# Performance work log

Measured on AMD Instinct MI355X. Metric: run time of the kernel, lower is better.

Reference implementation:

```python
import jax, jax.numpy as jnp
import numpy as np
from jax import lax

DIM = 256
HEADS = 8
P = 4  # split_size (patch_size)
SCALE = (DIM // HEADS) ** -0.5  # note: scale uses full head_dim = dim//heads, per the torch code


def _win(t, p1, p2, h):
    # 'b (h d) (gx p1) (gy p2) -> (b gx gy) h (p1 p2) d'
    b, c, X, Y = t.shape
    d = c // h
    gx, gy = X // p1, Y // p2
    t = t.reshape(b, h, d, gx, p1, gy, p2).transpose(0, 3, 5, 1, 4, 6, 2)
    return t.reshape(b * gx * gy, h, p1 * p2, d)


def _unwin(v, b, gx, gy, h, p1, p2):
    # '(b gx gy) h (p1 p2) d -> b (h d) (gx p1) (gy p2)'
    d = v.shape[-1]
    v = v.reshape(b, gx, gy, h, p1, p2, d).transpose(0, 3, 6, 1, 4, 2, 5)
    return v.reshape(b, h * d, gx * p1, gy * p2)


def _conv(x, w, stride):
    return lax.conv_general_dilated(x, w, stride, 'VALID',
                                    dimension_numbers=('NCHW', 'OIHW', 'NCHW'))


def _attn_branch(q, k, v, lepe):
    # q: (G,h,Nq,d), k/lepe: (G,h,Nk,d), v: (G,h,Nq,d)
    attn = jax.nn.softmax((q * SCALE) @ jnp.swapaxes(k, -2, -1), axis=-1)  # (G,h,Nq,Nk)
    # torch does attn.transpose(-2,-1) @ v + lepe -> output indexed by key tokens
    return jnp.einsum('ghqk,ghqd->ghkd', attn, v) + lepe


def setup_inputs() -> dict:
    key = jax.random.key(0)
    ks = jax.random.split(key, 6)
    b, x, y = 16, 64, 64
    fmap = jax.random.normal(ks[0], (b, DIM, x, y), dtype=jnp.float32)
    W_qvh = jax.random.normal(ks[1], (DIM, DIM // 2, 2, 1), dtype=jnp.float32) * 0.02
    W_qvv = jax.random.normal(ks[2], (DIM, DIM // 2, 1, 2), dtype=jnp.float32) * 0.02
    W_k = jax.random.normal(ks[3], (DIM, DIM), dtype=jnp.float32) * 0.02
    W_lepe = jax.random.normal(ks[4], (DIM, DIM), dtype=jnp.float32) * 0.02
    W_proj = jax.random.normal(ks[5], (DIM, DIM), dtype=jnp.float32) * 0.02
    return {"fmap": fmap, "W_qvh": W_qvh, "W_qvv": W_qvv,
            "W_k": W_k, "W_lepe": W_lepe, "W_proj": W_proj}


def reference(fmap, W_qvh, W_qvv, W_k, W_lepe, W_proj):
    b, n, x, y = fmap.shape
    h, p = HEADS, P
    half = n // 2
    # strided qv projections (size=0 path)
    qv_h = _conv(fmap[:, :half], W_qvh, (2, 1))  # (b, n, x/2, y)
    qv_v = _conv(fmap[:, half:], W_qvv, (1, 2))  # (b, n, x, y/2)
    # 1x1 convs as channel matmuls
    k_all = jnp.einsum('bcxy,oc->boxy', fmap, W_k)
    lepe_all = jnp.einsum('bcxy,oc->boxy', fmap, W_lepe)

    # horizontal branch: strips of width p spanning full height
    q_h = _win(qv_h[:, :half], x // 2, p, h)     # (b*(y/p), h, (x/2)*p, d)
    v_h = _win(qv_h[:, half:], x // 2, p, h)
    k_h = _win(k_all[:, :half], x, p, h)         # (b*(y/p), h, x*p, d)
    lepe_h = _win(lepe_all[:, :half], x, p, h)
    out_h = _attn_branch(q_h, k_h, v_h, lepe_h)  # (b*(y/p), h, x*p, d)
    out_h = _unwin(out_h, b, 1, y // p, h, x, p)  # (b, n/2, x, y)

    # vertical branch: strips of height p spanning full width
    q_v = _win(qv_v[:, :half], p, y // 2, h)
    v_v = _win(qv_v[:, half:], p, y // 2, h)
    k_v = _win(k_all[:, half:], p, y, h)
    lepe_v = _win(lepe_all[:, half:], p, y, h)
    out_v = _attn_branch(q_v, k_v, v_v, lepe_v)
    out_v = _unwin(out_v, b, x // p, 1, h, p, y)  # (b, n/2, x, y)

    cat = jnp.concatenate([out_h, out_v], axis=1)  # (b, n, x, y)
    return fmap + jnp.einsum('bcxy,oc->boxy', cat, W_proj)
```

## Files before the change

### kernel.cpp

```cpp
#include <hip/hip_runtime.h>
#include <hip/hip_bf16.h>

#define QSC 0.25503533f

typedef unsigned short bfu;
typedef unsigned int u32;
typedef __attribute__((ext_vector_type(8))) short bf8v;
typedef __attribute__((ext_vector_type(4))) float f32x4;
typedef __attribute__((ext_vector_type(8))) unsigned short u16x8;
typedef __attribute__((ext_vector_type(4))) unsigned int u32x4;

__device__ __forceinline__ bfu f2b(float x) {
    __hip_bfloat16 h = __float2bfloat16(x);
    return *(bfu*)&h;
}
__device__ __forceinline__ float bu2f(bfu u) {
    return __uint_as_float(((unsigned int)u) << 16);
}
__device__ __forceinline__ u32 cvtpk(float lo, float hi) {
    u32 r;
    asm("v_cvt_pk_bf16_f32 %0, %1, %2" : "=v"(r) : "v"(lo), "v"(hi));
    return r;
}
__device__ __forceinline__ void gload16(const bfu* g, bfu* l) {
    __builtin_amdgcn_global_load_lds(
        (const __attribute__((address_space(1))) unsigned int*)g,
        (__attribute__((address_space(3))) unsigned int*)l, 16, 0, 0);
}

__global__ __launch_bounds__(256) void k_prep_f(const float* __restrict__ fmap,
                                                bfu* __restrict__ Fbf) {
    const int x = blockIdx.x, b = blockIdx.y;
    const int t = threadIdx.x;
    __shared__ float tile[64][69];
    for (int cc = 0; cc < 256; cc += 64) {
        #pragma unroll
        for (int i = 0; i < 4; ++i) {
            const int c = (t >> 4) + i * 16, y4 = (t & 15) * 4;
            const float4 v = *(const float4*)(fmap + (((size_t)b * 256 + cc + c) * 64 + x) * 64 + y4);
            tile[y4][c] = v.x; tile[y4 + 1][c] = v.y; tile[y4 + 2][c] = v.z; tile[y4 + 3][c] = v.w;
        }
        __syncthreads();
        const int y = t >> 2, cs = (t & 3) * 16;
        u16x8 o0, o1;
        #pragma unroll
        for (int j = 0; j < 8; ++j) { o0[j] = f2b(tile[y][cs + j]); o1[j] = f2b(tile[y][cs + 8 + j]); }
        bfu* dst = Fbf + (((size_t)b * 64 + x) * 64 + y) * 256 + cc + cs;
        *(u16x8*)dst = o0; *(u16x8*)(dst + 8) = o1;
        __syncthreads();
    }
}

__global__ __launch_bounds__(256) void k_prep_w(
    const float* __restrict__ Wk, const float* __restrict__ Wl,
    const float* __restrict__ Wh, const float* __restrict__ Wv,
    bfu* __restrict__ Wkl, bfu* __restrict__ Whr, bfu* __restrict__ Wvr) {
    const int i = blockIdx.x * 256 + threadIdx.x;
    {
        const int o = i >> 8;
        Wkl[i] = f2b((o < 256) ? Wk[i] : Wl[i - 65536]);
    }
    if (i < 65536) {
        const int o = i >> 8, r = i & 255, kh = r >> 7, c = r & 127;
        const int s = (o * 128 + c) * 2 + kh;
        Whr[i] = f2b(Wh[s]);
        Wvr[i] = f2b(Wv[s]);
    }
}

template<int MODE>
__global__ __launch_bounds__(512) void k_gemm(
    const bfu* __restrict__ Ab16, const float* __restrict__ Af32,
    const bfu* __restrict__ Bsrc,
    bfu* __restrict__ o_kall, bfu* __restrict__ o_lepe, bfu* __restrict__ o_qv,
    const float* __restrict__ resid, float* __restrict__ outf) {
    const int ng = blockIdx.x, mt = blockIdx.y, b = blockIdx.z;
    const int m0 = mt * 128;
    const int t = threadIdx.x, lane = t & 63;
    const int wave = t >> 6;
    const int wm = wave >> 1, wn = wave & 1;
    const int lq = lane >> 4, lr = lane & 15;
    __shared__ bfu Bs[2][64 * 256];
    const bfu* fb = Bsrc + (size_t)b * 1048576;

    bf8v af[8][2];
    if (MODE == 3) {
        #pragma unroll
        for (int k0 = 0; k0 < 8; ++k0)
            #pragma unroll
            for (int mi = 0; mi < 2; ++mi) {
                const float* ap = Af32 + (size_t)(m0 + wm * 32 + mi * 16 + lr) * 256 + k0 * 32 + lq * 8;
                const float4 u0 = *(const float4*)ap;
                const float4 u1 = *(const float4*)(ap + 4);
                bf8v a;
                a[0] = (short)f2b(u0.x); a[1] = (short)f2b(u0.y);
                a[2] = (short)f2b(u0.z); a[3] = (short)f2b(u0.w);
                a[4] = (short)f2b(u1.x); a[5] = (short)f2b(u1.y);
                a[6] = (short)f2b(u1.z); a[7] = (short)f2b(u1.w);
                af[k0][mi] = a;
            }
    } else {
        #pragma unroll
        for (int k0 = 0; k0 < 8; ++k0)
            #pragma unroll
            for (int mi = 0; mi < 2; ++mi)
                af[k0][mi] = *(const bf8v*)(Ab16 + (size_t)(m0 + wm * 32 + mi * 16 + lr) * 256 + k0 * 32 + lq * 8);
    }

    auto stage = [&](int buf, int nt) {
        const int n0 = nt * 64;
        const int lrow = lane >> 5, c1 = lane & 31;
        #pragma unroll
        for (int i = 0; i < 4; ++i) {
            const int row = wave * 8 + i * 2 + lrow;
            const int cS = c1 ^ (row & 7);
            int so;
            if (MODE == 0 || MODE == 3) {
                so = (n0 + row) * 256 + cS * 8;
            } else if (MODE == 1) {
                const int n = n0 + row;
                const int xo = n >> 6, y = n & 63;
                so = ((2 * xo + (cS >> 4)) * 64 + y) * 256 + (cS & 15) * 8;
            } else {
                const int n = n0 + row;
                const int x = n >> 5, yo = n & 31;
                so = (x * 64 + 2 * yo + (cS >> 4)) * 256 + 128 + (cS & 15) * 8;
            }
            gload16(fb + so, &Bs[buf][(wave * 8 + i * 2) * 256]);
        }
    };

    const int nt0 = ng * 4;
    stage(0, nt0);
    __syncthreads();

    for (int tt = 0; tt < 4; ++tt) {
        if (tt + 1 < 4) stage((tt + 1) & 1, nt0 + tt + 1);

        const int buf = tt & 1;
        f32x4 acc[2][2];
        #pragma unroll
        for (int mi = 0; mi < 2; ++mi)
            #pragma unroll
            for (int ni = 0; ni < 2; ++ni) {
                acc[mi][ni][0] = 0.f; acc[mi][ni][1] = 0.f;
                acc[mi][ni][2] = 0.f; acc[mi][ni][3] = 0.f;
            }
        #pragma unroll
        for (int k0 = 0; k0 < 8; ++k0) {
            bf8v bv[2];
            #pragma unroll
            for (int ni = 0; ni < 2; ++ni) {
                const int row = wn * 32 + ni * 16 + lr;
                const int ck = (k0 * 4 + lq) ^ (row & 7);
                bv[ni] = *(const bf8v*)(&Bs[buf][row * 256 + ck * 8]);
            }
            #pragma unroll
            for (int mi = 0; mi < 2; ++mi)
                #pragma unroll
                for (int ni = 0; ni < 2; ++ni)
                    acc[mi][ni] = __builtin_amdgcn_mfma_f32_16x16x32_bf16(af[k0][mi], bv[ni], acc[mi][ni], 0, 0, 0);
        }

        const int n0 = (nt0 + tt) * 64;
        if (MODE == 0) {
            bfu* outp = (mt < 2) ? o_kall : o_lepe;
            const int chb = (mt & 1) * 128 + wm * 32;
            #pragma unroll
            for (int mi = 0; mi < 2; ++mi)
                #pragma unroll
                for (int ni = 0; ni < 2; ++ni) {
                    const int ch = chb + mi * 16 + lq * 4;
                    const int ngl = n0 + wn * 32 + ni * 16 + lr;
                    ushort4 pk;
                    pk.x = f2b(acc[mi][ni][0]); pk.y = f2b(acc[mi][ni][1]);
                    pk.z = f2b(acc[mi][ni][2]); pk.w = f2b(acc[mi][ni][3]);
                    *(ushort4*)(outp + ((size_t)b * 4096 + ngl) * 256 + ch) = pk;
                }
        } else if (MODE == 1 || MODE == 2) {
            const float qs = (mt == 0) ? QSC : 1.0f;
            #pragma unroll
            for (int mi = 0; mi < 2; ++mi)
                #pragma unroll
                for (int ni = 0; ni < 2; ++ni) {
                    const int ch = m0 + wm * 32 + mi * 16 + lq * 4;
                    const int ngl = n0 + wn * 32 + ni * 16 + lr;
                    ushort4 pk;
                    pk.x = f2b(acc[mi][ni][0] * qs); pk.y = f2b(acc[mi][ni][1] * qs);
                    pk.z = f2b(acc[mi][ni][2] * qs); pk.w = f2b(acc[mi][ni][3] * qs);
                    *(ushort4*)(o_qv + ((size_t)b * 2048 + ngl) * 256 + ch) = pk;
                }
        } else {
            #pragma unroll
            for (int mi = 0; mi < 2; ++mi)
                #pragma unroll
                for (int ni = 0; ni < 2; ++ni) {
                    const int ngl = n0 + wn * 32 + ni * 16 + lr;
                    #pragma unroll
                    for (int r = 0; r < 4; ++r) {
                        const int m = m0 + wm * 32 + mi * 16 + lq * 4 + r;
                        const size_t ad = ((size_t)b * 256 + m) * 4096 + ngl;
                        outf[ad] = resid[ad] + acc[mi][ni][r];
                    }
                }
        }
        if (tt + 1 < 4) __syncthreads();
    }
}

template<int BR>
__global__ __launch_bounds__(256) void k_attn(
    const bfu* __restrict__ Qv, const bfu* __restrict__ Kb,
    const bfu* __restrict__ Lp, bfu* __restrict__ cat) {
    const int bid = blockIdx.x;
    const int h = (bid >> 8) & 7;
    const int bg = bid & 255;
    const int b = bg >> 4, g = bg & 15;
    const int t = threadIdx.x, lane = t & 63, w = t >> 6;
    const int lr = lane & 15, lq = lane >> 4;
    const int chQ = h * 16, chV = 128 + h * 16;
    const int chO = (BR == 0) ? h * 16 : 128 + h * 16;
    const bfu* Qb = Qv + (size_t)b * 2048 * 256;
    const bfu* Kg = Kb + (size_t)b * 4096 * 256 + chO;
    const bfu* Lg = Lp + (size_t)b * 4096 * 256 + chO;
    bfu* Cg = cat + (size_t)b * 4096 * 256 + chO;

    __shared__ __align__(16) bfu q_lds[128 * 16];
    __shared__ __align__(16) bfu v_lds[128 * 16];
    __shared__ float psum[2][256];

    {
        const int tok = (w << 5) + (lane >> 1), half = lane & 1;
        const int sp = (BR == 0) ? ((tok >> 2) * 64 + g * 4 + (tok & 3))
                                 : ((g * 4 + (tok >> 5)) * 32 + (tok & 31));
        gload16(Qb + (size_t)sp * 256 + chQ + half * 8, q_lds + w * 512);
        gload16(Qb + (size_t)sp * 256 + chV + half * 8, v_lds + w * 512);
    }

    bf8v kf[4];
    #pragma unroll
    for (int ct = 0; ct < 4; ++ct) {
        const int ktok = (4 * w + ct) * 16 + lr;
        const int sp = (BR == 0) ? ((ktok >> 2) * 64 + g * 4 + (ktok & 3))
                                 : ((g * 4 + (ktok >> 6)) * 64 + (ktok & 63));
        if (lq < 2) kf[ct] = *(const bf8v*)(Kg + (size_t)sp * 256 + lq * 8);
        else        kf[ct] = bf8v{0, 0, 0, 0, 0, 0, 0, 0};
    }
    __syncthreads();

    f32x4 oacc[4];
    #pragma unroll
    for (int ct = 0; ct < 4; ++ct) { oacc[ct][0] = 0.f; oacc[ct][1] = 0.f; oacc[ct][2] = 0.f; oacc[ct][3] = 0.f; }

    for (int gq = 0; gq < 2; ++gq) {
        bf8v qf[4];
        #pragma unroll
        for (int qt = 0; qt < 4; ++qt) {
            const int qtok = gq * 64 + qt * 16 + lr;
            if (lq < 2) qf[qt] = *(const bf8v*)(q_lds + qtok * 16 + lq * 8);
            else        qf[qt] = bf8v{0, 0, 0, 0, 0, 0, 0, 0};
        }
        bf8v vf[2];
        #pragma unroll
        for (int c = 0; c < 2; ++c)
            #pragma unroll
            for (int j = 0; j < 8; ++j)
                vf[c][j] = (short)v_lds[(gq * 64 + c * 32 + lq * 8 + j) * 16 + lr];

        f32x4 acc[4][4];
        #pragma unroll
        for (int qt = 0; qt < 4; ++qt)
            #pragma unroll
            for (int ct = 0; ct < 4; ++ct) {
                acc[qt][ct][0] = 0.f; acc[qt][ct][1] = 0.f; acc[qt][ct][2] = 0.f; acc[qt][ct][3] = 0.f;
            }
        #pragma unroll
        for (int qt = 0; qt < 4; ++qt)
            #pragma unroll
            for (int ct = 0; ct < 4; ++ct)
                acc[qt][ct] = __builtin_amdgcn_mfma_f32_16x16x32_bf16(qf[qt], kf[ct], acc[qt][ct], 0, 0, 0);

        #pragma unroll
        for (int qt = 0; qt < 4; ++qt)
            #pragma unroll
            for (int ct = 0; ct < 4; ++ct)
                #pragma unroll
                for (int r = 0; r < 4; ++r)
                    acc[qt][ct][r] = exp2f(acc[qt][ct][r]);

        float rr[4][4];
        #pragma unroll
        for (int qt = 0; qt < 4; ++qt)
            #pragma unroll
            for (int r = 0; r < 4; ++r)
                rr[qt][r] = (acc[qt][0][r] + acc[qt][1][r]) + (acc[qt][2][r] + acc[qt][3][r]);
        #pragma unroll
        for (int s = 1; s <= 8; s <<= 1)
            #pragma unroll
            for (int qt = 0; qt < 4; ++qt)
                #pragma unroll
                for (int r = 0; r < 4; ++r)
                    rr[qt][r] += __shfl_xor(rr[qt][r], s);
        if (lr == 0) {
            #pragma unroll
            for (int qt = 0; qt < 4; ++qt)
                #pragma unroll
                for (int r = 0; r < 4; ++r)
                    psum[gq][w * 64 + qt * 16 + lq * 4 + r] = rr[qt][r];
        }
        __syncthreads();
        float inv[4][4];
        #pragma unroll
        for (int qt = 0; qt < 4; ++qt)
            #pragma unroll
            for (int r = 0; r < 4; ++r) {
                const int qi = qt * 16 + lq * 4 + r;
                inv[qt][r] = 1.0f / ((psum[gq][qi] + psum[gq][64 + qi]) +
                                     (psum[gq][128 + qi] + psum[gq][192 + qi]));
            }

        u32 pk[4][4][2];
        #pragma unroll
        for (int qt = 0; qt < 4; ++qt)
            #pragma unroll
            for (int ct = 0; ct < 4; ++ct) {
                pk[qt][ct][0] = cvtpk(acc[qt][ct][0] * inv[qt][0], acc[qt][ct][1] * inv[qt][1]);
                pk[qt][ct][1] = cvtpk(acc[qt][ct][2] * inv[qt][2], acc[qt][ct][3] * inv[qt][3]);
            }

        const int base = ((lane >> 4) & 1) * 32 + (lane & 15);
        const bool hi = (lq >= 2);
        #pragma unroll
        for (int c = 0; c < 2; ++c) {
            #pragma unroll
            for (int ct = 0; ct < 4; ++ct) {
                const u32 a0 = (u32)__shfl((int)pk[2 * c][ct][0], base);
                const u32 a1 = (u32)__shfl((int)pk[2 * c][ct][1], base);
                const u32 a2 = (u32)__shfl((int)pk[2 * c][ct][0], base + 16);
                const u32 a3 = (u32)__shfl((int)pk[2 * c][ct][1], base + 16);
                const u32 b0 = (u32)__shfl((int)pk[2 * c + 1][ct][0], base);
                const u32 b1 = (u32)__shfl((int)pk[2 * c + 1][ct][1], base);
                const u32 b2 = (u32)__shfl((int)pk[2 * c + 1][ct][0], base + 16);
                const u32 b3 = (u32)__shfl((int)pk[2 * c + 1][ct][1], base + 16);
                u32x4 wd;
                wd[0] = hi ? b0 : a0; wd[1] = hi ? b1 : a1;
                wd[2] = hi ? b2 : a2; wd[3] = hi ? b3 : a3;
                const bf8v pf = __builtin_bit_cast(bf8v, wd);
                oacc[ct] = __builtin_amdgcn_mfma_f32_16x16x32_bf16(vf[c], pf, oacc[ct], 0, 0, 0);
            }
        }
    }

    #pragma unroll
    for (int ct = 0; ct < 4; ++ct) {
        const int ktok = (4 * w + ct) * 16 + lr;
        const int sp = (BR == 0) ? ((ktok >> 2) * 64 + g * 4 + (ktok & 3))
                                 : ((g * 4 + (ktok >> 6)) * 64 + (ktok & 63));
        const size_t off = (size_t)sp * 256 + lq * 4;
        const ushort4 l4 = *(const ushort4*)(Lg + off);
        ushort4 o;
        o.x = f2b(oacc[ct][0] + bu2f(l4.x));
        o.y = f2b(oacc[ct][1] + bu2f(l4.y));
        o.z = f2b(oacc[ct][2] + bu2f(l4.z));
        o.w = f2b(oacc[ct][3] + bu2f(l4.w));
        *(ushort4*)(Cg + off) = o;
    }
}

extern "C" void kernel_launch(void* const* d_in, const int* in_sizes, int n_in,
                              void* d_out, int out_size, void* d_ws, size_t ws_size,
                              hipStream_t stream) {
    const float* fmap = (const float*)d_in[0];
    const float* Wqvh = (const float*)d_in[1];
    const float* Wqvv = (const float*)d_in[2];
    const float* Wk   = (const float*)d_in[3];
    const float* Wl   = (const float*)d_in[4];
    const float* Wp   = (const float*)d_in[5];
    float* out = (float*)d_out;
    char* ws = (char*)d_ws;

    bfu* Fbf   = (bfu*)(ws);
    bfu* cat   = Fbf;
    bfu* k_all = (bfu*)(ws + 33554432);
    bfu* lepe  = (bfu*)(ws + 67108864);
    bfu* qvh   = (bfu*)(ws + 100663296);
    bfu* qvv   = (bfu*)(ws + 117440512);

    bfu* Wkl = (bfu*)d_out;
    bfu* Whr = (bfu*)((char*)d_out + 262144);
    bfu* Wvr = (bfu*)((char*)d_out + 393216);

    k_prep_f<<<dim3(64, 16), 256, 0, stream>>>(fmap, Fbf);
    k_prep_w<<<dim3(512), 256, 0, stream>>>(Wk, Wl, Wqvh, Wqvv, Wkl, Whr, Wvr);
    k_gemm<0><<<dim3(16, 4, 16), 512, 0, stream>>>(Wkl, nullptr, Fbf, k_all, lepe, nullptr, nullptr, nullptr);
    k_gemm<1><<<dim3(8, 2, 16), 512, 0, stream>>>(Whr, nullptr, Fbf, nullptr, nullptr, qvh, nullptr, nullptr);
    k_gemm<2><<<dim3(8, 2, 16), 512, 0, stream>>>(Wvr, nullptr, Fbf, nullptr, nullptr, qvv, nullptr, nullptr);
    k_attn<0><<<dim3(2048), 256, 0, stream>>>(qvh, k_all, lepe, cat);
    k_attn<1><<<dim3(2048), 256, 0, stream>>>(qvv, k_all, lepe, cat);
    k_gemm<3><<<dim3(16, 2, 16), 512, 0, stream>>>(nullptr, Wp, cat, nullptr, nullptr, nullptr, fmap, out);
}
```

Baseline: 233.2 us.

## Run attention blocks as single wavefronts with K staged in LDS

The attention kernel now uses one 64-thread wavefront per (batch, strip, head) instead of four. Each wave loads all 256 keys into LDS and loops over 8 query groups of 16, keeping 16 output accumulators. This removes the cross-wave softmax partial-sum exchange and its block barriers, and trims the wasted lane work in the P·V MFMA packing. In exchange, each block does four times the serial work, register pressure rises from holding 16 score tiles, and the number of waves in flight drops.

Measured after the change: 216.7 us. 1.08x faster.

```diff
diff --git a/kernel.cpp b/kernel.cpp
--- a/kernel.cpp
+++ b/kernel.cpp
@@ -209,14 +209,14 @@
 }
 
 template<int BR>
-__global__ __launch_bounds__(256) void k_attn(
+__global__ __launch_bounds__(64, 2) void k_attn(
     const bfu* __restrict__ Qv, const bfu* __restrict__ Kb,
     const bfu* __restrict__ Lp, bfu* __restrict__ cat) {
     const int bid = blockIdx.x;
-    const int h = (bid >> 8) & 7;
+    const int h = bid >> 8;
     const int bg = bid & 255;
     const int b = bg >> 4, g = bg & 15;
-    const int t = threadIdx.x, lane = t & 63, w = t >> 6;
+    const int lane = threadIdx.x;
     const int lr = lane & 15, lq = lane >> 4;
     const int chQ = h * 16, chV = 128 + h * 16;
     const int chO = (BR == 0) ? h * 16 : 128 + h * 16;
@@ -225,135 +225,101 @@
     const bfu* Lg = Lp + (size_t)b * 4096 * 256 + chO;
     bfu* Cg = cat + (size_t)b * 4096 * 256 + chO;
 
-    __shared__ __align__(16) bfu q_lds[128 * 16];
-    __shared__ __align__(16) bfu v_lds[128 * 16];
-    __shared__ float psum[2][256];
+    __shared__ __align__(16) bfu q_lds[2048];
+    __shared__ __align__(16) bfu v_lds[2048];
+    __shared__ __align__(16) bfu k_lds[4096];
 
     {
-        const int tok = (w << 5) + (lane >> 1), half = lane & 1;
-        const int sp = (BR == 0) ? ((tok >> 2) * 64 + g * 4 + (tok & 3))
-                                 : ((g * 4 + (tok >> 5)) * 32 + (tok & 31));
-        gload16(Qb + (size_t)sp * 256 + chQ + half * 8, q_lds + w * 512);
-        gload16(Qb + (size_t)sp * 256 + chV + half * 8, v_lds + w * 512);
-    }
-
-    bf8v kf[4];
+        const int half = lane & 1;
+        #pragma unroll
+        for (int c = 0; c < 4; ++c) {
+            const int tok = c * 32 + (lane >> 1);
+            const int sp = (BR == 0) ? ((tok >> 2) * 64 + g * 4 + (tok & 3))
+                                     : ((g * 4 + (tok >> 5)) * 32 + (tok & 31));
+            gload16(Qb + (size_t)sp * 256 + chQ + half * 8, q_lds + c * 512);
+            gload16(Qb + (size_t)sp * 256 + chV + half * 8, v_lds + c * 512);
+        }
+        #pragma unroll
+        for (int c = 0; c < 8; ++c) {
+            const int ktok = c * 32 + (lane >> 1);
+            const int sp = (BR == 0) ? ((ktok >> 2) * 64 + g * 4 + (ktok & 3))
+                                     : ((g * 4 + (ktok >> 6)) * 64 + (ktok & 63));
+            gload16(Kg + (size_t)sp * 256 + half * 8, k_lds + c * 512);
+        }
+    }
+    __syncthreads();
+
+    const bf8v zero8 = {0, 0, 0, 0, 0, 0, 0, 0};
+    const f32x4 zero4 = {0.f, 0.f, 0.f, 0.f};
+    const bool hi = (lq >= 2);
+    const int base = (lq & 1) * 32 + lr;
+
+    f32x4 oacc[16];
     #pragma unroll
-    for (int ct = 0; ct < 4; ++ct) {
-        const int ktok = (4 * w + ct) * 16 + lr;
-        const int sp = (BR == 0) ? ((ktok >> 2) * 64 + g * 4 + (ktok & 3))
-                                 : ((g * 4 + (ktok >> 6)) * 64 + (ktok & 63));
-        if (lq < 2) kf[ct] = *(const bf8v*)(Kg + (size_t)sp * 256 + lq * 8);
-        else        kf[ct] = bf8v{0, 0, 0, 0, 0, 0, 0, 0};
-    }
-    __syncthreads();
-
-    f32x4 oacc[4];
+    for (int ct = 0; ct < 16; ++ct) {
+        oacc[ct][0] = 0.f; oacc[ct][1] = 0.f; oacc[ct][2] = 0.f; oacc[ct][3] = 0.f;
+    }
+
+    for (int qg = 0; qg < 8; ++qg) {
+        const bf8v qf = hi ? zero8 : *(const bf8v*)(q_lds + (qg * 16 + lr) * 16 + lq * 8);
+        bf8v vf;
+        #pragma unroll
+        for (int j = 0; j < 8; ++j)
+            vf[j] = (short)v_lds[(qg * 16 + (lq & 1) * 8 + j) * 16 + lr];
+
+        f32x4 acc[16];
+        #pragma unroll
+        for (int ct = 0; ct < 16; ++ct) {
+            const bf8v kf = hi ? zero8 : *(const bf8v*)(k_lds + (ct * 16 + lr) * 16 + lq * 8);
+            acc[ct] = __builtin_amdgcn_mfma_f32_16x16x32_bf16(qf, kf, zero4, 0, 0, 0);
+        }
+
+        #pragma unroll
+        for (int ct = 0; ct < 16; ++ct)
+            #pragma unroll
+            for (int r = 0; r < 4; ++r)
+                acc[ct][r] = exp2f(acc[ct][r]);
+
+        float rr[4];
+        #pragma unroll
+        for (int r = 0; r < 4; ++r) {
+            float s = 0.f;
+            #pragma unroll
+            for (int ct = 0; ct < 16; ++ct) s += acc[ct][r];
+            rr[r] = s;
+        }
+        #pragma unroll
+        for (int s = 1; s <= 8; s <<= 1)
+            #pragma unroll
+            for (int r = 0; r < 4; ++r)
+                rr[r] += __shfl_xor(rr[r], s);
+        float inv[4];
+        #pragma unroll
+        for (int r = 0; r < 4; ++r) inv[r] = 1.0f / rr[r];
+
+        u32 pk[16][2];
+        #pragma unroll
+        for (int ct = 0; ct < 16; ++ct) {
+            pk[ct][0] = cvtpk(acc[ct][0] * inv[0], acc[ct][1] * inv[1]);
+            pk[ct][1] = cvtpk(acc[ct][2] * inv[2], acc[ct][3] * inv[3]);
+        }
+        #pragma unroll
+        for (int ct = 0; ct < 16; ++ct) {
+            const u32 a0 = (u32)__shfl((int)pk[ct][0], base);
+            const u32 a1 = (u32)__shfl((int)pk[ct][1], base);
+            const u32 a2 = (u32)__shfl((int)pk[ct][0], base + 16);
+            const u32 a3 = (u32)__shfl((int)pk[ct][1], base + 16);
+            u32x4 wd;
+            wd[0] = hi ? 0u : a0; wd[1] = hi ? 0u : a1;
+            wd[2] = hi ? 0u : a2; wd[3] = hi ? 0u : a3;
+            const bf8v pf = __builtin_bit_cast(bf8v, wd);
+            oacc[ct] = __builtin_amdgcn_mfma_f32_16x16x32_bf16(vf, pf, oacc[ct], 0, 0, 0);
+        }
+    }
+
     #pragma unroll
-    for (int ct = 0; ct < 4; ++ct) { oacc[ct][0] = 0.f; oacc[ct][1] = 0.f; oacc[ct][2] = 0.f; oacc[ct][3] = 0.f; }
-
-    for (int gq = 0; gq < 2; ++gq) {
-        bf8v qf[4];
-        #pragma unroll
-        for (int qt = 0; qt < 4; ++qt) {
-            const int qtok = gq * 64 + qt * 16 + lr;
-            if (lq < 2) qf[qt] = *(const bf8v*)(q_lds + qtok * 16 + lq * 8);
-            else        qf[qt] = bf8v{0, 0, 0, 0, 0, 0, 0, 0};
-        }
-        bf8v vf[2];
-        #pragma unroll
-        for (int c = 0; c < 2; ++c)
-            #pragma unroll
-            for (int j = 0; j < 8; ++j)
-                vf[c][j] = (short)v_lds[(gq * 64 + c * 32 + lq * 8 + j) * 16 + lr];
-
-        f32x4 acc[4][4];
-        #pragma unroll
-        for (int qt = 0; qt < 4; ++qt)
-            #pragma unroll
-            for (int ct = 0; ct < 4; ++ct) {
-                acc[qt][ct][0] = 0.f; acc[qt][ct][1] = 0.f; acc[qt][ct][2] = 0.f; acc[qt][ct][3] = 0.f;
-            }
-        #pragma unroll
-        for (int qt = 0; qt < 4; ++qt)
-            #pragma unroll
-            for (int ct = 0; ct < 4; ++ct)
-                acc[qt][ct] = __builtin_amdgcn_mfma_f32_16x16x32_bf16(qf[qt], kf[ct], acc[qt][ct], 0, 0, 0);
-
-        #pragma unroll
-        for (int qt = 0; qt < 4; ++qt)
-            #pragma unroll
-            for (int ct = 0; ct < 4; ++ct)
-                #pragma unroll
-                for (int r = 0; r < 4; ++r)
-                    acc[qt][ct][r] = exp2f(acc[qt][ct][r]);
-
-        float rr[4][4];
-        #pragma unroll
-        for (int qt = 0; qt < 4; ++qt)
-            #pragma unroll
-            for (int r = 0; r < 4; ++r)
-                rr[qt][r] = (acc[qt][0][r] + acc[qt][1][r]) + (acc[qt][2][r] + acc[qt][3][r]);
-        #pragma unroll
-        for (int s = 1; s <= 8; s <<= 1)
-            #pragma unroll
-            for (int qt = 0; qt < 4; ++qt)
-                #pragma unroll
-                for (int r = 0; r < 4; ++r)
-                    rr[qt][r] += __shfl_xor(rr[qt][r], s);
-        if (lr == 0) {
-            #pragma unroll
-            for (int qt = 0; qt < 4; ++qt)
-                #pragma unroll
-                for (int r = 0; r < 4; ++r)
-                    psum[gq][w * 64 + qt * 16 + lq * 4 + r] = rr[qt][r];
-        }
-        __syncthreads();
-        float inv[4][4];
-        #pragma unroll
-        for (int qt = 0; qt < 4; ++qt)
-            #pragma unroll
-            for (int r = 0; r < 4; ++r) {
-                const int qi = qt * 16 + lq * 4 + r;
-                inv[qt][r] = 1.0f / ((psum[gq][qi] + psum[gq][64 + qi]) +
-                                     (psum[gq][128 + qi] + psum[gq][192 + qi]));
-            }
-
-        u32 pk[4][4][2];
-        #pragma unroll
-        for (int qt = 0; qt < 4; ++qt)
-            #pragma unroll
-            for (int ct = 0; ct < 4; ++ct) {
-                pk[qt][ct][0] = cvtpk(acc[qt][ct][0] * inv[qt][0], acc[qt][ct][1] * inv[qt][1]);
-                pk[qt][ct][1] = cvtpk(acc[qt][ct][2] * inv[qt][2], acc[qt][ct][3] * inv[qt][3]);
-            }
-
-        const int base = ((lane >> 4) & 1) * 32 + (lane & 15);
-        const bool hi = (lq >= 2);
-        #pragma unroll
-        for (int c = 0; c < 2; ++c) {
-            #pragma unroll
-            for (int ct = 0; ct < 4; ++ct) {
-                const u32 a0 = (u32)__shfl((int)pk[2 * c][ct][0], base);
-                const u32 a1 = (u32)__shfl((int)pk[2 * c][ct][1], base);
-                const u32 a2 = (u32)__shfl((int)pk[2 * c][ct][0], base + 16);
-                const u32 a3 = (u32)__shfl((int)pk[2 * c][ct][1], base + 16);
-                const u32 b0 = (u32)__shfl((int)pk[2 * c + 1][ct][0], base);
-                const u32 b1 = (u32)__shfl((int)pk[2 * c + 1][ct][1], base);
-                const u32 b2 = (u32)__shfl((int)pk[2 * c + 1][ct][0], base + 16);
-                const u32 b3 = (u32)__shfl((int)pk[2 * c + 1][ct][1], base + 16);
-                u32x4 wd;
-                wd[0] = hi ? b0 : a0; wd[1] = hi ? b1 : a1;
-                wd[2] = hi ? b2 : a2; wd[3] = hi ? b3 : a3;
-                const bf8v pf = __builtin_bit_cast(bf8v, wd);
-                oacc[ct] = __builtin_amdgcn_mfma_f32_16x16x32_bf16(vf[c], pf, oacc[ct], 0, 0, 0);
-            }
-        }
-    }
-
-    #pragma unroll
-    for (int ct = 0; ct < 4; ++ct) {
-        const int ktok = (4 * w + ct) * 16 + lr;
+    for (int ct = 0; ct < 16; ++ct) {
+        const int ktok = ct * 16 + lr;
         const int sp = (BR == 0) ? ((ktok >> 2) * 64 + g * 4 + (ktok & 3))
                                  : ((g * 4 + (ktok >> 6)) * 64 + (ktok & 63));
         const size_t off = (size_t)sp * 256 + lq * 4;
@@ -395,7 +361,7 @@
     k_gemm<0><<<dim3(16, 4, 16), 512, 0, stream>>>(Wkl, nullptr, Fbf, k_all, lepe, nullptr, nullptr, nullptr);
     k_gemm<1><<<dim3(8, 2, 16), 512, 0, stream>>>(Whr, nullptr, Fbf, nullptr, nullptr, qvh, nullptr, nullptr);
     k_gemm<2><<<dim3(8, 2, 16), 512, 0, stream>>>(Wvr, nullptr, Fbf, nullptr, nullptr, qvv, nullptr, nullptr);
-    k_attn<0><<<dim3(2048), 256, 0, stream>>>(qvh, k_all, lepe, cat);
-    k_attn<1><<<dim3(2048), 256, 0, stream>>>(qvv, k_all, lepe, cat);
+    k_attn<0><<<dim3(2048), 64, 0, stream>>>(qvh, k_all, lepe, cat);
+    k_attn<1><<<dim3(2048), 64, 0, stream>>>(qvv, k_all, lepe, cat);
     k_gemm<3><<<dim3(16, 2, 16), 512, 0, stream>>>(nullptr, Wp, cat, nullptr, nullptr, nullptr, fmap, out);
 }
```
